# Kernel optimization log

Hardware: AMD Instinct MI355X
Metric: run time of the kernel (lower is better)

## Reference

```python
import jax, jax.numpy as jnp
import numpy as np

T, H, I, E, K = 4096, 2048, 768, 64, 8  # tokens, hidden, moe_intermediate, experts, top_k


def setup_inputs() -> dict:
    key = jax.random.key(0)
    k1, k2, k3, k4 = jax.random.split(key, 4)
    return {
        "x": jax.random.normal(k1, (T, H), jnp.float32),
        "gate_w": jax.random.normal(k2, (E, H), jnp.float32) * 0.02,          # router weight [E, H]
        "w_gate_up": jax.random.normal(k3, (E, H, 2 * I), jnp.float32) * 0.02,  # stacked gate|up [E, H, 2I]
        "w_down": jax.random.normal(k4, (E, I, H), jnp.float32) * 0.02,        # stacked down [E, I, H]
        "top_k": K,
    }


def reference(x, gate_w, w_gate_up, w_down, top_k):
    n_tok, hidden = x.shape
    n_exp = gate_w.shape[0]
    inter = w_down.shape[1]

    # Router: softmax over experts (fp32 for stability), top-k, renormalize (norm_topk_prob)
    logits = x @ gate_w.T                                   # [T, E]
    probs = jax.nn.softmax(logits.astype(jnp.float32), axis=-1)
    top_p, top_i = jax.lax.top_k(probs, top_k)              # [T, K]
    top_p = top_p / jnp.sum(top_p, axis=-1, keepdims=True)

    # Scatter top-k weights into dense combine matrix [T, E] (top_k indices are distinct)
    combine = jnp.zeros((n_tok, n_exp), jnp.float32)
    combine = combine.at[jnp.arange(n_tok)[:, None], top_i].set(top_p)
    combine = combine.astype(x.dtype)

    # Per-expert SwiGLU MLP, accumulated via scan over the (fixed) expert axis.
    def body(acc, ws):
        wgu, wd, cw = ws                                    # [H,2I], [I,H], [T]
        gu = x @ wgu                                        # [T, 2I]
        h = jax.nn.silu(gu[:, :inter]) * gu[:, inter:]      # [T, I]
        return acc + (h @ wd) * cw[:, None], None

    out, _ = jax.lax.scan(body, jnp.zeros_like(x), (w_gate_up, w_down, combine.T))
    return out
```

## Files before the change

kernel.cpp:

```cpp
#include <hip/hip_runtime.h>
#include <hip/hip_bf16.h>
#include <cstdint>
#include <cstddef>

#define T_TOK 4096
#define HID   2048
#define INTER 768
#define NEXP  64

typedef float  f32x4  __attribute__((ext_vector_type(4)));
typedef __bf16 bf16x8 __attribute__((ext_vector_type(8)));
typedef __bf16 bf16x4 __attribute__((ext_vector_type(4)));

__device__ __forceinline__ void gl16(const void* g, void* l) {
  __builtin_amdgcn_global_load_lds((const __attribute__((address_space(1))) void*)g,
                                   (__attribute__((address_space(3))) void*)l, 16, 0, 0);
}

#define BAR() do { asm volatile("" ::: "memory"); __builtin_amdgcn_s_barrier(); asm volatile("" ::: "memory"); } while (0)


__global__ void zero_meta_kernel(int* counts, int* fill) {
  int t = threadIdx.x;
  if (t < NEXP) { counts[t] = 0; fill[t] = 0; }
}

__global__ void scan_kernel(const int* __restrict__ counts, int* __restrict__ offsets,
                            int* __restrict__ tb) {
  if (threadIdx.x == 0) {
    int s = 0, ts = 0;
    for (int e = 0; e < NEXP; e++) {
      offsets[e] = s; tb[e] = ts;
      s += counts[e]; ts += (counts[e] + 255) >> 8;
    }
    offsets[NEXP] = s; tb[NEXP] = ts;
  }
}

__global__ void scatter_kernel(const int* __restrict__ topk_id, const float* __restrict__ topk_w,
                               const int* __restrict__ offsets, int* __restrict__ fill,
                               int* __restrict__ pair_tok, float* __restrict__ pair_w,
                               int* __restrict__ pair_pos) {
  int i = blockIdx.x * 256 + threadIdx.x;
  int e = topk_id[i];
  int pos = offsets[e] + atomicAdd(&fill[e], 1);
  pair_tok[pos] = i >> 3;
  pair_w[pos]  = topk_w[i];
  pair_pos[i]  = pos;
}


__device__ __forceinline__ void transpose_tile(
    const float* __restrict__ src, __bf16* __restrict__ dst,
    int Kd, int Nd, int mode, int wid, char* Sw, int lane) {
  const int g = lane >> 4, nq = lane & 15;
  const int NT = Nd >> 6, KT = Kd >> 6, NB = Nd >> 7;
  int tpe = KT * NT;
  int e = wid / tpe;
  int rem = wid - e * tpe;
  int kt = rem / NT;
  int nt = rem - kt * NT;
  const float* sp = src + ((size_t)e * Kd + (size_t)kt * 64) * Nd + nt * 64;

  float4 vv[16];
  #pragma unroll
  for (int kq = 0; kq < 16; kq++)
    vv[kq] = *(const float4*)(sp + (size_t)(kq * 4 + g) * Nd + nq * 4);

  const int n_l = nq * 4 + g;
  #pragma unroll
  for (int kq = 0; kq < 16; kq++) {
    float4 v = vv[kq];
    float t0 = __shfl_xor(v.x, 32), t1 = __shfl_xor(v.y, 32);
    float t2 = __shfl_xor(v.z, 32), t3 = __shfl_xor(v.w, 32);
    bool hi2 = (g & 2) != 0;
    float a0 = hi2 ? t2 : v.x, a1 = hi2 ? t3 : v.y;
    float a2 = hi2 ? v.z : t0, a3 = hi2 ? v.w : t1;
    float s0 = __shfl_xor(a0, 16), s1 = __shfl_xor(a1, 16);
    float s2 = __shfl_xor(a2, 16), s3 = __shfl_xor(a3, 16);
    bool odd = (g & 1) != 0;
    float u0 = odd ? s1 : a0, u1 = odd ? a1 : s0;
    float u2 = odd ? s3 : a2, u3 = odd ? a3 : s2;
    bf16x4 b; b[0] = (__bf16)u0; b[1] = (__bf16)u1; b[2] = (__bf16)u2; b[3] = (__bf16)u3;
    *(bf16x4*)(Sw + n_l * 128 + ((kq ^ (n_l & 15)) << 3)) = b;
  }
  asm volatile("s_waitcnt lgkmcnt(0)" ::: "memory");
  __builtin_amdgcn_sched_barrier(0);

  if (mode == 0) {
    uint4* gdst = (uint4*)dst + ((((size_t)e * NB + (nt >> 1)) * KT + kt) << 10) + ((nt & 1) << 6) + lane;
    #pragma unroll
    for (int q = 0; q < 8; q++) {
      int p0 = (2 * q) ^ (lane & 15), p1 = (2 * q + 1) ^ (lane & 15);
      uint2 lo = *(const uint2*)(Sw + lane * 128 + (p0 << 3));
      uint2 hi = *(const uint2*)(Sw + lane * 128 + (p1 << 3));
      gdst[q * 128] = make_uint4(lo.x, lo.y, hi.x, hi.y);
    }
  } else {
    int n = nt * 64 + lane;
    int isup = (n >= INTER) ? 1 : 0;
    int hcol = isup ? n - INTER : n;
    int nb = hcol >> 7, ho = hcol & 127;
    int rp = isup * 128 + ho;
    uint4* gdst = (uint4*)dst + ((((size_t)e * 6 + nb) * KT + kt) << 11) + rp;
    #pragma unroll
    for (int q = 0; q < 8; q++) {
      int p0 = (2 * q) ^ (lane & 15), p1 = (2 * q + 1) ^ (lane & 15);
      uint2 lo = *(const uint2*)(Sw + lane * 128 + (p0 << 3));
      uint2 hi = *(const uint2*)(Sw + lane * 128 + (p1 << 3));
      gdst[q * 256] = make_uint4(lo.x, lo.y, hi.x, hi.y);
    }
  }
}


__global__ __launch_bounds__(256) void fat1_kernel(
    const float* __restrict__ x, const float* __restrict__ gw, __bf16* __restrict__ xbf,
    int* __restrict__ topk_id, float* __restrict__ topk_w, int* __restrict__ counts,
    const float* __restrict__ wgu, __bf16* __restrict__ w2gu) {
  __shared__ __align__(16) char fsm[32768];
  const int tid = threadIdx.x, lane = tid & 63, wv = tid >> 6;

  if (blockIdx.x >= 256) {
    transpose_tile(wgu, w2gu, HID, 2 * INTER, 1,
                   ((int)blockIdx.x - 256) * 4 + wv, fsm + wv * 8192, lane);
    return;
  }

  float (*gs)[65] = (float (*)[65])fsm;
  float (*xs)[65] = (float (*)[65])(fsm + 16640);
  const int tblk = blockIdx.x * 16;

  float acc[4] = {0.f, 0.f, 0.f, 0.f};
  for (int kc = 0; kc < HID; kc += 64) {
    #pragma unroll
    for (int i = 0; i < 4; i++) {
      int r = tid >> 2;
      int c = (tid & 3) * 16 + i * 4;
      float4 v = *(const float4*)(gw + (size_t)r * HID + kc + c);
      gs[r][c + 0] = v.x; gs[r][c + 1] = v.y; gs[r][c + 2] = v.z; gs[r][c + 3] = v.w;
    }
    {
      int r = tid >> 4;
      int c = (tid & 15) * 4;
      float4 v = *(const float4*)(x + (size_t)(tblk + r) * HID + kc + c);
      xs[r][c + 0] = v.x; xs[r][c + 1] = v.y; xs[r][c + 2] = v.z; xs[r][c + 3] = v.w;
      bf16x4 b;
      b[0] = (__bf16)v.x; b[1] = (__bf16)v.y; b[2] = (__bf16)v.z; b[3] = (__bf16)v.w;
      *(bf16x4*)(xbf + (size_t)(tblk + r) * HID + kc + c) = b;
    }
    __syncthreads();
    #pragma unroll 8
    for (int k = 0; k < 64; k++) {
      float g = gs[lane][k];
      #pragma unroll
      for (int j = 0; j < 4; j++) acc[j] = fmaf(xs[wv * 4 + j][k], g, acc[j]);
    }
    __syncthreads();
  }

  for (int j = 0; j < 4; j++) {
    int t = tblk + wv * 4 + j;
    float vsel = acc[j];
    float m1 = 0.f, denom = 0.f;
    int myid = 0; float myw = 0.f;
    for (int s = 0; s < 8; s++) {
      float bv = vsel; int bi = lane;
      #pragma unroll
      for (int off = 32; off > 0; off >>= 1) {
        float ov = __shfl_xor(bv, off);
        int   oi = __shfl_xor(bi, off);
        if (ov > bv || (ov == bv && oi < bi)) { bv = ov; bi = oi; }
      }
      if (s == 0) m1 = bv;
      float ev = __expf(bv - m1);
      denom += ev;
      if (lane == s)  { myid = bi; myw = ev; }
      if (lane == bi) vsel = -3.402823466e38f;
    }
    if (lane < 8) {
      topk_id[t * 8 + lane] = myid;
      topk_w[t * 8 + lane]  = myw / denom;
      atomicAdd(&counts[myid], 1);
    }
  }
}


__global__ __launch_bounds__(512, 2) void fat2_kernel(
    const uint4* __restrict__ xbf4, const uint4* __restrict__ w2gu,
    const int* __restrict__ offsets, const int* __restrict__ tb,
    const int* __restrict__ pair_tok, const float* __restrict__ pair_w,
    uint4* __restrict__ H2,
    const float* __restrict__ wd, __bf16* __restrict__ w2d, int nwgG1) {
  __shared__ __align__(16) char smem[81920];
  const int tid = threadIdx.x, lane = tid & 63, w = tid >> 6;
  const int bid = blockIdx.x;

  if (bid >= nwgG1) {
    transpose_tile(wd, w2d, INTER, HID, 0,
                   (bid - nwgG1) * 8 + w, smem + w * 8192, lane);
    return;
  }

  const int q8 = nwgG1 >> 3, r8 = nwgG1 & 7;
  const int xcd = bid & 7, idx = bid >> 3;
  const int wg = (xcd < r8 ? xcd * (q8 + 1) : r8 * (q8 + 1) + (xcd - r8) * q8) + idx;
  const int mt0 = wg % 3, t1 = wg / 3, nb = t1 % 6, e = t1 / 6;
  const int off = offsets[e], cnt = offsets[e + 1] - off;
  const uint4* Bb = w2gu + (size_t)(e * 6 + nb) * 65536;
  const int wm = w >> 2, wn = w & 3;
  const int g = lane >> 4, nq = lane & 15;
  const int sq = w >> 1, sr = w & 1;
  const int aoff  = (sq << 12) + (sr << 11);
  const int boffg = (sq << 8) + (sr << 6);

#define STA1(s, ks) gl16(rA1 + (size_t)(ks) * 4, smem + (s) * 16384 + aoff + (lane << 4))
#define STA2(s, ks) gl16(rA2 + (size_t)(ks) * 4, smem + (s) * 16384 + aoff + 1024 + (lane << 4))
#define STBG(pb, ks) gl16(Bb + (size_t)(ks) * 1024 + boffg + lane, \
                          smem + 49152 + (pb) * 16384 + (boffg << 4) + (lane << 4))
#define STBU(pb, ks) gl16(Bb + (size_t)(ks) * 1024 + boffg + 128 + lane, \
                          smem + 49152 + (pb) * 16384 + ((boffg + 128) << 4) + (lane << 4))

  for (int mt = mt0; mt * 256 < cnt; mt += 3) {
    const int rows = min(256, cnt - mt * 256);
    const int m0 = mt * 256;
    const int rm = rows - 1;
    const int tok1 = pair_tok[off + m0 + min(sr * 128 + lane, rm)];
    const int tok2 = pair_tok[off + m0 + min(sr * 128 + 64 + lane, rm)];
    const uint4* rA1 = xbf4 + (size_t)tok1 * 256 + sq;
    const uint4* rA2 = xbf4 + (size_t)tok2 * 256 + sq;

    f32x4 ag[8][2], au[8][2];
    #pragma unroll
    for (int i = 0; i < 8; i++)
      #pragma unroll
      for (int j = 0; j < 2; j++)
        #pragma unroll
        for (int q = 0; q < 4; q++) { ag[i][j][q] = 0.f; au[i][j][q] = 0.f; }

    STA1(0, 0); STA2(0, 0); STBG(0, 0); STBU(0, 0); STA1(1, 1); STA2(1, 1);
    for (int ks = 0; ks < 64; ks++) {
      char* bA = smem + (ks % 3) * 16384;
      char* bB = smem + 49152 + (ks & 1) * 16384;
      bf16x8 af[4], bg[2], bu[2];
      if (ks < 63) asm volatile("s_waitcnt vmcnt(3)" ::: "memory");
      else         asm volatile("s_waitcnt vmcnt(1)" ::: "memory");
      BAR();
      if (ks + 1 < 64) STBG((ks + 1) & 1, ks + 1);
      #pragma unroll
      for (int mi = 0; mi < 4; mi++)
        af[mi] = *(const bf16x8*)(bA + (g << 12) + ((wm * 128 + mi * 16 + nq) << 4));
      #pragma unroll
      for (int ni = 0; ni < 2; ni++)
        bg[ni] = *(const bf16x8*)(bB + (g << 12) + ((wn * 32 + ni * 16 + nq) << 4));
      __builtin_amdgcn_s_setprio(1);
      #pragma unroll
      for (int mi = 0; mi < 4; mi++)
        #pragma unroll
        for (int ni = 0; ni < 2; ni++)
          ag[mi][ni] = __builtin_amdgcn_mfma_f32_16x16x32_bf16(af[mi], bg[ni], ag[mi][ni], 0, 0, 0);
      __builtin_amdgcn_s_setprio(0);
      if (ks < 63) asm volatile("s_waitcnt vmcnt(3)" ::: "memory");
      else         asm volatile("s_waitcnt vmcnt(0)" ::: "memory");
      BAR();
      if (ks + 1 < 64) STBU((ks + 1) & 1, ks + 1);
      #pragma unroll
      for (int ni = 0; ni < 2; ni++)
        bu[ni] = *(const bf16x8*)(bB + (g << 12) + ((128 + wn * 32 + ni * 16 + nq) << 4));
      __builtin_amdgcn_s_setprio(1);
      #pragma unroll
      for (int mi = 0; mi < 4; mi++)
        #pragma unroll
        for (int ni = 0; ni < 2; ni++)
          au[mi][ni] = __builtin_amdgcn_mfma_f32_16x16x32_bf16(af[mi], bu[ni], au[mi][ni], 0, 0, 0);
      __builtin_amdgcn_s_setprio(0);
      BAR();
      if (ks + 2 < 64) STA1((ks + 2) % 3, ks + 2);
      #pragma unroll
      for (int mi = 0; mi < 4; mi++)
        af[mi] = *(const bf16x8*)(bA + (g << 12) + ((wm * 128 + 64 + mi * 16 + nq) << 4));
      __builtin_amdgcn_s_setprio(1);
      #pragma unroll
      for (int mi = 0; mi < 4; mi++)
        #pragma unroll
        for (int ni = 0; ni < 2; ni++)
          ag[4 + mi][ni] = __builtin_amdgcn_mfma_f32_16x16x32_bf16(af[mi], bg[ni], ag[4 + mi][ni], 0, 0, 0);
      __builtin_amdgcn_s_setprio(0);
      BAR();
      if (ks + 2 < 64) STA2((ks + 2) % 3, ks + 2);
      __builtin_amdgcn_s_setprio(1);
      #pragma unroll
      for (int mi = 0; mi < 4; mi++)
        #pragma unroll
        for (int ni = 0; ni < 2; ni++)
          au[4 + mi][ni] = __builtin_amdgcn_mfma_f32_16x16x32_bf16(af[mi], bu[ni], au[4 + mi][ni], 0, 0, 0);
      __builtin_amdgcn_s_setprio(0);
    }

    #pragma unroll
    for (int mi = 0; mi < 8; mi++) {
      const int mrow = (mi < 4) ? (wm * 128 + mi * 16) : (wm * 128 + 64 + (mi - 4) * 16);
      #pragma unroll
      for (int reg = 0; reg < 4; reg++) {
        int rrow = mrow + g * 4 + reg;
        float pw = (rrow < rows) ? pair_w[off + m0 + rrow] : 0.f;
        #pragma unroll
        for (int ni = 0; ni < 2; ni++) {
          float gv = ag[mi][ni][reg];
          float uv = au[mi][ni][reg];
          float sv = gv / (1.f + __expf(-gv));
          int col = wn * 32 + ni * 16 + nq;
          *(__bf16*)(smem + rrow * 256 + ((col * 2) ^ ((rrow & 7) << 4))) = (__bf16)(sv * uv * pw);
        }
      }
    }
    BAR();
    {
      uint4* Hb = H2 + (size_t)(tb[e] + mt) * 24576 + nb * 16 * 256;
      #pragma unroll
      for (int i = 0; i < 8; i++) {
        int idx2 = tid + i * 512;
        int gx = idx2 >> 8, row = idx2 & 255;
        uint4 v = *(const uint4*)(smem + row * 256 + ((gx * 16) ^ ((row & 7) << 4)));
        Hb[gx * 256 + row] = v;
      }
    }
    BAR();
  }
#undef STA1
#undef STA2
#undef STBG
#undef STBU
}


__global__ __launch_bounds__(512, 2) void gemm2_kernel(
    const uint4* __restrict__ H2, const uint4* __restrict__ w2d,
    const int* __restrict__ offsets, const int* __restrict__ tb,
    __bf16* __restrict__ ybuf, int e0, int nwg) {
  __shared__ __align__(16) char smem[131072];
  const int bid = blockIdx.x;
  const int q8 = nwg >> 3, r8 = nwg & 7;
  const int xcd = bid & 7, idx = bid >> 3;
  const int wg = (xcd < r8 ? xcd * (q8 + 1) : r8 * (q8 + 1) + (xcd - r8) * q8) + idx;
  const int mt0 = wg % 3, t1 = wg / 3, nb2 = t1 % 8, ez = t1 / 8;
  const int e = e0 + ez;
  const int off = offsets[e], cnt = offsets[e + 1] - off;
  const uint4* Bw = w2d;
  const int pnl0 = ez * 16 + nb2 * 2, pnl1 = pnl0 + 1;
  const int tid = threadIdx.x, lane = tid & 63, w = tid >> 6;
  const int wm = w >> 2, wn = w & 3;
  const int g = lane >> 4, nq = lane & 15;

#define S2A1(p, ks) do { size_t so_ = (size_t)(ks) * 2048 + (w << 8);            \
    char* d_ = smem + (p) * 65536 + (w << 12);                                   \
    gl16(Ab + so_ + lane,       d_ + (lane << 4));                               \
    gl16(Ab + so_ + 128 + lane, d_ + ((128 + lane) << 4)); } while (0)
#define S2A2(p, ks) do { size_t so_ = (size_t)(ks) * 2048 + (w << 8);            \
    char* d_ = smem + (p) * 65536 + (w << 12);                                   \
    gl16(Ab + so_ + 64 + lane,  d_ + ((64 + lane) << 4));                        \
    gl16(Ab + so_ + 192 + lane, d_ + ((192 + lane) << 4)); } while (0)
#define S2BG(p, ks) do { size_t so_ = ((size_t)pnl0 * 12 + (ks)) * 1024 + (w << 7); \
    char* d_ = smem + (p) * 65536 + 32768 + (w << 12);                           \
    gl16(Bw + so_ + lane,      d_ + (lane << 4));                                \
    gl16(Bw + so_ + 64 + lane, d_ + ((64 + lane) << 4)); } while (0)
#define S2BH(p, ks) do { size_t so_ = ((size_t)pnl1 * 12 + (ks)) * 1024 + (w << 7); \
    char* d_ = smem + (p) * 65536 + 32768 + (w << 12);                           \
    gl16(Bw + so_ + lane,      d_ + ((128 + lane) << 4));                        \
    gl16(Bw + so_ + 64 + lane, d_ + ((192 + lane) << 4)); } while (0)

  for (int mt = mt0; mt * 256 < cnt; mt += 3) {
    const int rows = min(256, cnt - mt * 256);
    const uint4* Ab = H2 + (size_t)(tb[e] + mt) * 24576;

    f32x4 a0[8][2], a1[8][2];
    #pragma unroll
    for (int i = 0; i < 8; i++)
      #pragma unroll
      for (int j = 0; j < 2; j++)
        #pragma unroll
        for (int q = 0; q < 4; q++) { a0[i][j][q] = 0.f; a1[i][j][q] = 0.f; }

    S2A1(0, 0); S2BG(0, 0); S2BH(0, 0); S2A2(0, 0);
    for (int ks = 0; ks < 12; ks++) {
      const int p = ks & 1;
      char* bA = smem + p * 65536;
      char* bB = bA + 32768;
      const bool pre = (ks + 1 < 12);
      bf16x8 af[4][2], bl[2][2], bh[2][2];
      asm volatile("s_waitcnt vmcnt(4)" ::: "memory");
      BAR();
      if (pre) S2A1(p ^ 1, ks + 1);
      #pragma unroll
      for (int kk = 0; kk < 2; kk++) {
        const int q = kk * 4 + g;
        #pragma unroll
        for (int mi = 0; mi < 4; mi++)
          af[mi][kk] = *(const bf16x8*)(bA + (q << 12) + ((wm * 128 + mi * 16 + nq) << 4));
        #pragma unroll
        for (int ni = 0; ni < 2; ni++)
          bl[ni][kk] = *(const bf16x8*)(bB + (q << 12) + ((wn * 32 + ni * 16 + nq) << 4));
      }
      __builtin_amdgcn_s_setprio(1);
      #pragma unroll
      for (int kk = 0; kk < 2; kk++)
        #pragma unroll
        for (int mi = 0; mi < 4; mi++)
          #pragma unroll
          for (int ni = 0; ni < 2; ni++)
            a0[mi][ni] = __builtin_amdgcn_mfma_f32_16x16x32_bf16(af[mi][kk], bl[ni][kk], a0[mi][ni], 0, 0, 0);
      __builtin_amdgcn_s_setprio(0);
      if (pre) asm volatile("s_waitcnt vmcnt(4)" ::: "memory");
      else     asm volatile("s_waitcnt vmcnt(2)" ::: "memory");
      BAR();
      if (pre) S2BG(p ^ 1, ks + 1);
      #pragma unroll
      for (int kk = 0; kk < 2; kk++) {
        const int q = kk * 4 + g;
        #pragma unroll
        for (int ni = 0; ni < 2; ni++)
          bh[ni][kk] = *(const bf16x8*)(bB + (q << 12) + ((128 + wn * 32 + ni * 16 + nq) << 4));
      }
      __builtin_amdgcn_s_setprio(1);
      #pragma unroll
      for (int kk = 0; kk < 2; kk++)
        #pragma unroll
        for (int mi = 0; mi < 4; mi++)
          #pragma unroll
          for (int ni = 0; ni < 2; ni++)
            a1[mi][ni] = __builtin_amdgcn_mfma_f32_16x16x32_bf16(af[mi][kk], bh[ni][kk], a1[mi][ni], 0, 0, 0);
      __builtin_amdgcn_s_setprio(0);
      if (pre) asm volatile("s_waitcnt vmcnt(4)" ::: "memory");
      else     asm volatile("s_waitcnt vmcnt(0)" ::: "memory");
      BAR();
      if (pre) S2BH(p ^ 1, ks + 1);
      #pragma unroll
      for (int kk = 0; kk < 2; kk++) {
        const int q = kk * 4 + g;
        #pragma unroll
        for (int mi = 0; mi < 4; mi++)
          af[mi][kk] = *(const bf16x8*)(bA + (q << 12) + ((wm * 128 + 64 + mi * 16 + nq) << 4));
      }
      __builtin_amdgcn_s_setprio(1);
      #pragma unroll
      for (int kk = 0; kk < 2; kk++)
        #pragma unroll
        for (int mi = 0; mi < 4; mi++)
          #pragma unroll
          for (int ni = 0; ni < 2; ni++)
            a0[4 + mi][ni] = __builtin_amdgcn_mfma_f32_16x16x32_bf16(af[mi][kk], bl[ni][kk], a0[4 + mi][ni], 0, 0, 0);
      __builtin_amdgcn_s_setprio(0);
      BAR();
      if (pre) S2A2(p ^ 1, ks + 1);
      __builtin_amdgcn_s_setprio(1);
      #pragma unroll
      for (int kk = 0; kk < 2; kk++)
        #pragma unroll
        for (int mi = 0; mi < 4; mi++)
          #pragma unroll
          for (int ni = 0; ni < 2; ni++)
            a1[4 + mi][ni] = __builtin_amdgcn_mfma_f32_16x16x32_bf16(af[mi][kk], bh[ni][kk], a1[4 + mi][ni], 0, 0, 0);
      __builtin_amdgcn_s_setprio(0);
    }

    const int m0 = mt * 256;
    #pragma unroll
    for (int mi = 0; mi < 8; mi++) {
      const int mrow = (mi < 4) ? (wm * 128 + mi * 16) : (wm * 128 + 64 + (mi - 4) * 16);
      #pragma unroll
      for (int reg = 0; reg < 4; reg++) {
        int rrow = mrow + g * 4 + reg;
        if (rrow < rows) {
          __bf16* yrow = ybuf + (size_t)(off + m0 + rrow) * HID + nb2 * 256 + wn * 32;
          #pragma unroll
          for (int ni = 0; ni < 2; ni++) {
            yrow[ni * 16 + nq]       = (__bf16)a0[mi][ni][reg];
            yrow[128 + ni * 16 + nq] = (__bf16)a1[mi][ni][reg];
          }
        }
      }
    }
  }
#undef S2A1
#undef S2A2
#undef S2BG
#undef S2BH
}


__global__ __launch_bounds__(256) void reduce_kernel(
    const __bf16* __restrict__ ybuf, const int* __restrict__ pair_pos,
    float* __restrict__ out) {
  const int t = blockIdx.x, j = threadIdx.x;
  const int* pp = pair_pos + t * 8;
  float s[8] = {0.f, 0.f, 0.f, 0.f, 0.f, 0.f, 0.f, 0.f};
  #pragma unroll
  for (int k = 0; k < 8; k++) {
    bf16x8 v = *(const bf16x8*)(ybuf + (size_t)pp[k] * HID + j * 8);
    #pragma unroll
    for (int c = 0; c < 8; c++) s[c] += (float)v[c];
  }
  float4 o0 = make_float4(s[0], s[1], s[2], s[3]);
  float4 o1 = make_float4(s[4], s[5], s[6], s[7]);
  *(float4*)(out + (size_t)t * HID + j * 8) = o0;
  *(float4*)(out + (size_t)t * HID + j * 8 + 4) = o1;
}


extern "C" void kernel_launch(void* const* d_in, const int* in_sizes, int n_in,
                              void* d_out, int out_size, void* d_ws, size_t ws_size,
                              hipStream_t stream) {
  const float* x   = (const float*)d_in[0];
  const float* gw  = (const float*)d_in[1];
  const float* wgu = (const float*)d_in[2];
  const float* wd  = (const float*)d_in[3];
  float* out = (float*)d_out;

  char* ws = (char*)d_ws;
  int*   counts   = (int*)(ws + 0);
  int*   fill     = (int*)(ws + 256);
  int*   offsets  = (int*)(ws + 512);
  int*   tb       = (int*)(ws + 1024);
  int*   topk_id  = (int*)(ws + 4096);
  float* topk_w   = (float*)(ws + 135168);
  int*   pair_tok = (int*)(ws + 266240);
  float* pair_w   = (float*)(ws + 397312);
  int*   pair_pos = (int*)(ws + 528384);
  __bf16* xbf  = (__bf16*)(ws + 1048576);
  __bf16* ybuf = (__bf16*)(ws + 68157440);
  uint4*  H2   = (uint4*)(ws + 537919488);
  const size_t w2_base = 613416960ull;
  __bf16* w2gu = (__bf16*)(ws + w2_base);
  __bf16* w2d  = (__bf16*)(ws + w2_base + 64ull * 6291456ull);

  zero_meta_kernel<<<1, 128, 0, stream>>>(counts, fill);
  fat1_kernel<<<256 + 12288, 256, 0, stream>>>(x, gw, xbf, topk_id, topk_w, counts, wgu, w2gu);
  scan_kernel<<<1, 64, 0, stream>>>(counts, offsets, tb);
  scatter_kernel<<<128, 256, 0, stream>>>(topk_id, topk_w, offsets, fill, pair_tok, pair_w, pair_pos);

  fat2_kernel<<<1152 + 3072, 512, 0, stream>>>((const uint4*)xbf, (const uint4*)w2gu,
                                               offsets, tb, pair_tok, pair_w, H2,
                                               wd, w2d, 1152);
  gemm2_kernel<<<1536, 512, 0, stream>>>(H2, (const uint4*)w2d, offsets, tb, ybuf, 0, 1536);
  reduce_kernel<<<T_TOK, 256, 0, stream>>>(ybuf, pair_pos, out);
}
```

Measured before the change: 900.4 us.

## Halve gemm2 K-step and use triple-buffered A with double-buffered B in LDS

Restructures the gemm2 main loop from 12 K-steps of 64 to 24 K-steps of 32. A tiles move to a three-stage ring prefetched two steps ahead, and B tiles stay double-buffered. LDS use drops from 128KB to 80KB, and the B panel addressing is changed to match. The goal is deeper prefetch of the activation tiles and less shared memory per block, at the cost of twice as many barriers and waitcnt points per K.

```diff
diff --git a/kernel.cpp b/kernel.cpp
--- a/kernel.cpp
+++ b/kernel.cpp
@@ -339,7 +339,7 @@
     const uint4* __restrict__ H2, const uint4* __restrict__ w2d,
     const int* __restrict__ offsets, const int* __restrict__ tb,
     __bf16* __restrict__ ybuf, int e0, int nwg) {
-  __shared__ __align__(16) char smem[131072];
+  __shared__ __align__(16) char smem[81920];
   const int bid = blockIdx.x;
   const int q8 = nwg >> 3, r8 = nwg & 7;
   const int xcd = bid & 7, idx = bid >> 3;
@@ -347,28 +347,23 @@
   const int mt0 = wg % 3, t1 = wg / 3, nb2 = t1 % 8, ez = t1 / 8;
   const int e = e0 + ez;
   const int off = offsets[e], cnt = offsets[e + 1] - off;
-  const uint4* Bw = w2d;
-  const int pnl0 = ez * 16 + nb2 * 2, pnl1 = pnl0 + 1;
+  const int pnl0 = ez * 16 + nb2 * 2;
+  const uint4* B0 = w2d + (size_t)pnl0 * 12288;
+  const uint4* B1 = B0 + 12288;
   const int tid = threadIdx.x, lane = tid & 63, w = tid >> 6;
   const int wm = w >> 2, wn = w & 3;
   const int g = lane >> 4, nq = lane & 15;
-
-#define S2A1(p, ks) do { size_t so_ = (size_t)(ks) * 2048 + (w << 8);            \
-    char* d_ = smem + (p) * 65536 + (w << 12);                                   \
-    gl16(Ab + so_ + lane,       d_ + (lane << 4));                               \
-    gl16(Ab + so_ + 128 + lane, d_ + ((128 + lane) << 4)); } while (0)
-#define S2A2(p, ks) do { size_t so_ = (size_t)(ks) * 2048 + (w << 8);            \
-    char* d_ = smem + (p) * 65536 + (w << 12);                                   \
-    gl16(Ab + so_ + 64 + lane,  d_ + ((64 + lane) << 4));                        \
-    gl16(Ab + so_ + 192 + lane, d_ + ((192 + lane) << 4)); } while (0)
-#define S2BG(p, ks) do { size_t so_ = ((size_t)pnl0 * 12 + (ks)) * 1024 + (w << 7); \
-    char* d_ = smem + (p) * 65536 + 32768 + (w << 12);                           \
-    gl16(Bw + so_ + lane,      d_ + (lane << 4));                                \
-    gl16(Bw + so_ + 64 + lane, d_ + ((64 + lane) << 4)); } while (0)
-#define S2BH(p, ks) do { size_t so_ = ((size_t)pnl1 * 12 + (ks)) * 1024 + (w << 7); \
-    char* d_ = smem + (p) * 65536 + 32768 + (w << 12);                           \
-    gl16(Bw + so_ + lane,      d_ + ((128 + lane) << 4));                        \
-    gl16(Bw + so_ + 64 + lane, d_ + ((192 + lane) << 4)); } while (0)
+  const int sq = w >> 1, sr = w & 1;
+  const int aoff = (sq << 12) + (sr << 11);
+
+#define S2A1(s, ks) gl16(Ab + (size_t)(ks) * 1024 + (sq << 8) + (sr << 7) + lane, \
+                         smem + (s) * 16384 + aoff + (lane << 4))
+#define S2A2(s, ks) gl16(Ab + (size_t)(ks) * 1024 + (sq << 8) + (sr << 7) + 64 + lane, \
+                         smem + (s) * 16384 + aoff + 1024 + (lane << 4))
+#define S2BG(pb, ks) gl16(B0 + (size_t)(ks) * 512 + (sq << 7) + (sr << 6) + lane, \
+                          smem + 49152 + (pb) * 16384 + (sq << 12) + (sr << 10) + (lane << 4))
+#define S2BH(pb, ks) gl16(B1 + (size_t)(ks) * 512 + (sq << 7) + (sr << 6) + lane, \
+                          smem + 49152 + (pb) * 16384 + (sq << 12) + 2048 + (sr << 10) + (lane << 4))
 
   for (int mt = mt0; mt * 256 < cnt; mt += 3) {
     const int rows = min(256, cnt - mt * 256);
@@ -382,85 +377,62 @@
         #pragma unroll
         for (int q = 0; q < 4; q++) { a0[i][j][q] = 0.f; a1[i][j][q] = 0.f; }
 
-    S2A1(0, 0); S2BG(0, 0); S2BH(0, 0); S2A2(0, 0);
-    for (int ks = 0; ks < 12; ks++) {
-      const int p = ks & 1;
-      char* bA = smem + p * 65536;
-      char* bB = bA + 32768;
-      const bool pre = (ks + 1 < 12);
-      bf16x8 af[4][2], bl[2][2], bh[2][2];
-      asm volatile("s_waitcnt vmcnt(4)" ::: "memory");
-      BAR();
-      if (pre) S2A1(p ^ 1, ks + 1);
-      #pragma unroll
-      for (int kk = 0; kk < 2; kk++) {
-        const int q = kk * 4 + g;
-        #pragma unroll
-        for (int mi = 0; mi < 4; mi++)
-          af[mi][kk] = *(const bf16x8*)(bA + (q << 12) + ((wm * 128 + mi * 16 + nq) << 4));
-        #pragma unroll
-        for (int ni = 0; ni < 2; ni++)
-          bl[ni][kk] = *(const bf16x8*)(bB + (q << 12) + ((wn * 32 + ni * 16 + nq) << 4));
-      }
-      __builtin_amdgcn_s_setprio(1);
-      #pragma unroll
-      for (int kk = 0; kk < 2; kk++)
-        #pragma unroll
-        for (int mi = 0; mi < 4; mi++)
-          #pragma unroll
-          for (int ni = 0; ni < 2; ni++)
-            a0[mi][ni] = __builtin_amdgcn_mfma_f32_16x16x32_bf16(af[mi][kk], bl[ni][kk], a0[mi][ni], 0, 0, 0);
-      __builtin_amdgcn_s_setprio(0);
-      if (pre) asm volatile("s_waitcnt vmcnt(4)" ::: "memory");
-      else     asm volatile("s_waitcnt vmcnt(2)" ::: "memory");
-      BAR();
-      if (pre) S2BG(p ^ 1, ks + 1);
-      #pragma unroll
-      for (int kk = 0; kk < 2; kk++) {
-        const int q = kk * 4 + g;
-        #pragma unroll
-        for (int ni = 0; ni < 2; ni++)
-          bh[ni][kk] = *(const bf16x8*)(bB + (q << 12) + ((128 + wn * 32 + ni * 16 + nq) << 4));
-      }
-      __builtin_amdgcn_s_setprio(1);
-      #pragma unroll
-      for (int kk = 0; kk < 2; kk++)
-        #pragma unroll
-        for (int mi = 0; mi < 4; mi++)
-          #pragma unroll
-          for (int ni = 0; ni < 2; ni++)
-            a1[mi][ni] = __builtin_amdgcn_mfma_f32_16x16x32_bf16(af[mi][kk], bh[ni][kk], a1[mi][ni], 0, 0, 0);
-      __builtin_amdgcn_s_setprio(0);
-      if (pre) asm volatile("s_waitcnt vmcnt(4)" ::: "memory");
-      else     asm volatile("s_waitcnt vmcnt(0)" ::: "memory");
-      BAR();
-      if (pre) S2BH(p ^ 1, ks + 1);
-      #pragma unroll
-      for (int kk = 0; kk < 2; kk++) {
-        const int q = kk * 4 + g;
-        #pragma unroll
-        for (int mi = 0; mi < 4; mi++)
-          af[mi][kk] = *(const bf16x8*)(bA + (q << 12) + ((wm * 128 + 64 + mi * 16 + nq) << 4));
-      }
-      __builtin_amdgcn_s_setprio(1);
-      #pragma unroll
-      for (int kk = 0; kk < 2; kk++)
-        #pragma unroll
-        for (int mi = 0; mi < 4; mi++)
-          #pragma unroll
-          for (int ni = 0; ni < 2; ni++)
-            a0[4 + mi][ni] = __builtin_amdgcn_mfma_f32_16x16x32_bf16(af[mi][kk], bl[ni][kk], a0[4 + mi][ni], 0, 0, 0);
-      __builtin_amdgcn_s_setprio(0);
-      BAR();
-      if (pre) S2A2(p ^ 1, ks + 1);
-      __builtin_amdgcn_s_setprio(1);
-      #pragma unroll
-      for (int kk = 0; kk < 2; kk++)
-        #pragma unroll
-        for (int mi = 0; mi < 4; mi++)
-          #pragma unroll
-          for (int ni = 0; ni < 2; ni++)
-            a1[4 + mi][ni] = __builtin_amdgcn_mfma_f32_16x16x32_bf16(af[mi][kk], bh[ni][kk], a1[4 + mi][ni], 0, 0, 0);
+    S2A1(0, 0); S2A2(0, 0); S2BG(0, 0); S2BH(0, 0); S2A1(1, 1); S2A2(1, 1);
+    for (int ks = 0; ks < 24; ks++) {
+      char* bA = smem + (ks % 3) * 16384;
+      char* bB = smem + 49152 + (ks & 1) * 16384;
+      bf16x8 af[4], bl[2], bh[2];
+      if (ks < 23) asm volatile("s_waitcnt vmcnt(3)" ::: "memory");
+      else         asm volatile("s_waitcnt vmcnt(1)" ::: "memory");
+      BAR();
+      if (ks + 1 < 24) S2BG((ks + 1) & 1, ks + 1);
+      #pragma unroll
+      for (int mi = 0; mi < 4; mi++)
+        af[mi] = *(const bf16x8*)(bA + (g << 12) + ((wm * 128 + mi * 16 + nq) << 4));
+      #pragma unroll
+      for (int ni = 0; ni < 2; ni++)
+        bl[ni] = *(const bf16x8*)(bB + (g << 12) + ((wn * 32 + ni * 16 + nq) << 4));
+      __builtin_amdgcn_s_setprio(1);
+      #pragma unroll
+      for (int mi = 0; mi < 4; mi++)
+        #pragma unroll
+        for (int ni = 0; ni < 2; ni++)
+          a0[mi][ni] = __builtin_amdgcn_mfma_f32_16x16x32_bf16(af[mi], bl[ni], a0[mi][ni], 0, 0, 0);
+      __builtin_amdgcn_s_setprio(0);
+      if (ks < 23) asm volatile("s_waitcnt vmcnt(3)" ::: "memory");
+      else         asm volatile("s_waitcnt vmcnt(0)" ::: "memory");
+      BAR();
+      if (ks + 1 < 24) S2BH((ks + 1) & 1, ks + 1);
+      #pragma unroll
+      for (int ni = 0; ni < 2; ni++)
+        bh[ni] = *(const bf16x8*)(bB + (g << 12) + ((128 + wn * 32 + ni * 16 + nq) << 4));
+      __builtin_amdgcn_s_setprio(1);
+      #pragma unroll
+      for (int mi = 0; mi < 4; mi++)
+        #pragma unroll
+        for (int ni = 0; ni < 2; ni++)
+          a1[mi][ni] = __builtin_amdgcn_mfma_f32_16x16x32_bf16(af[mi], bh[ni], a1[mi][ni], 0, 0, 0);
+      __builtin_amdgcn_s_setprio(0);
+      BAR();
+      if (ks + 2 < 24) S2A1((ks + 2) % 3, ks + 2);
+      #pragma unroll
+      for (int mi = 0; mi < 4; mi++)
+        af[mi] = *(const bf16x8*)(bA + (g << 12) + ((wm * 128 + 64 + mi * 16 + nq) << 4));
+      __builtin_amdgcn_s_setprio(1);
+      #pragma unroll
+      for (int mi = 0; mi < 4; mi++)
+        #pragma unroll
+        for (int ni = 0; ni < 2; ni++)
+          a0[4 + mi][ni] = __builtin_amdgcn_mfma_f32_16x16x32_bf16(af[mi], bl[ni], a0[4 + mi][ni], 0, 0, 0);
+      __builtin_amdgcn_s_setprio(0);
+      BAR();
+      if (ks + 2 < 24) S2A2((ks + 2) % 3, ks + 2);
+      __builtin_amdgcn_s_setprio(1);
+      #pragma unroll
+      for (int mi = 0; mi < 4; mi++)
+        #pragma unroll
+        for (int ni = 0; ni < 2; ni++)
+          a1[4 + mi][ni] = __builtin_amdgcn_mfma_f32_16x16x32_bf16(af[mi], bh[ni], a1[4 + mi][ni], 0, 0, 0);
       __builtin_amdgcn_s_setprio(0);
     }
 
```

Result: no change. 896.1 us, median of 2 (-0.5%).
